# Kernel optimization log

Measured on AMD Instinct MI355X. Metric: run time of the kernel, lower is better.

Reference implementation:

```python
import jax, jax.numpy as jnp
import numpy as np

N = 50000
E = 800000
D = 128
C = 16


def setup_inputs() -> dict:
    key = jax.random.key(0)
    ks = jax.random.split(key, 16)
    inp = {
        "src": jax.random.randint(ks[0], (E,), 0, N),
        "dst": jax.random.randint(ks[1], (E,), 0, N),
        "inputs": jax.random.normal(ks[2], (N, D), dtype=jnp.float32),
        "edge_weights": jax.random.uniform(ks[3], (E,), dtype=jnp.float32),
    }
    s = 1.0 / np.sqrt(D)
    for i, k in zip(range(1, 5), ks[4:8]):
        inp[f"W{i}"] = jax.random.uniform(k, (D, D), jnp.float32, -s, s)
        inp[f"b{i}"] = jnp.zeros((D,), jnp.float32)
    inp["Wr"] = jax.random.uniform(ks[8], (D, D), jnp.float32, -s, s)
    inp["br"] = jnp.zeros((D,), jnp.float32)
    inp["Wo"] = jax.random.uniform(ks[9], (D, C), jnp.float32, -s, s)
    inp["bo"] = jnp.zeros((C,), jnp.float32)
    return inp


def _graph_conv(x, W, b, src, dst, ew, inv_sqrt_out, inv_sqrt_in):
    # DGL GraphConv, norm='both': scale src by out_deg^-1/2, weighted SpMM, scale by in_deg^-1/2
    h = (x * inv_sqrt_out[:, None]) @ W            # [N, d_out]
    m = h[src] * ew[:, None]                       # gather + edge scale, [E, d_out]
    agg = jax.ops.segment_sum(m, dst, num_segments=N)
    return agg * inv_sqrt_in[:, None] + b


def reference(src, dst, inputs, edge_weights, W1, b1, W2, b2, W3, b3, W4, b4, Wr, br, Wo, bo):
    ones = jnp.ones((E,), jnp.float32)
    deg_out = jnp.clip(jax.ops.segment_sum(ones, src, num_segments=N), 1.0)
    deg_in = jnp.clip(jax.ops.segment_sum(ones, dst, num_segments=N), 1.0)
    iso = jax.lax.rsqrt(deg_out)
    isi = jax.lax.rsqrt(deg_in)

    res = inputs @ Wr + br
    out = jax.nn.relu(_graph_conv(inputs, W1, b1, src, dst, edge_weights, iso, isi))
    out = jax.nn.relu(_graph_conv(out, W2, b2, src, dst, edge_weights, iso, isi))
    out = jax.nn.relu(_graph_conv(out, W3, b3, src, dst, edge_weights, iso, isi))
    out = _graph_conv(out, W4, b4, src, dst, edge_weights, iso, isi)
    out = jax.nn.relu(out + res)
    return out @ Wo + bo
```

## Files before the change

kernel.cpp:

```cpp
#include <hip/hip_runtime.h>

#define NN 50000
#define EE 800000
#define DD 128
#define CC 16
#define HCOPIES 64
#define NRANGE 16384

typedef __attribute__((ext_vector_type(8))) short bf16x8;
typedef __attribute__((ext_vector_type(4))) float f32x4;

__device__ inline unsigned short f2bf(float x) {
    unsigned int u = __float_as_uint(x);
    unsigned int r = (u + 0x7FFFu + ((u >> 16) & 1u)) >> 16;
    return (unsigned short)r;
}
__device__ inline float bf2f(unsigned short h) {
    return __uint_as_float(((unsigned int)h) << 16);
}

__global__ __launch_bounds__(256) void k_hist_lds(
        const int* __restrict__ src, const int* __restrict__ dst,
        unsigned int* __restrict__ hist) {
    __shared__ unsigned int lds[NRANGE];
    const int t = threadIdx.x;
    const int r = blockIdx.x / HCOPIES;
    const int sub = blockIdx.x % HCOPIES;
    const int base = r * NRANGE;
    const int hi = min(base + NRANGE, NN) - base;

    for (int i = t; i < NRANGE; i += 256) lds[i] = 0;
    __syncthreads();

    const int chunk = EE / HCOPIES;
    const int e0 = sub * chunk;
    const int e1 = e0 + chunk;
    for (int e = e0 + t; e < e1; e += 256) {
        int s = src[e];
        int d = dst[e];
        unsigned us = (unsigned)(s - base);
        unsigned ud = (unsigned)(d - base);
        if (us < (unsigned)hi) atomicAdd(&lds[us], 1u);
        if (ud < (unsigned)hi) atomicAdd(&lds[ud], 0x10000u);
    }
    __syncthreads();

    for (int i = t; i < hi; i += 256) hist[(size_t)sub * NN + base + i] = lds[i];
}

__global__ void k_reduce_deg(const unsigned int* __restrict__ hist,
                             int* __restrict__ cd,
                             float* __restrict__ iso, float* __restrict__ isi) {
    int i = blockIdx.x * blockDim.x + threadIdx.x;
    if (i < NN) {
        unsigned int sum = 0;
#pragma unroll
        for (int c = 0; c < HCOPIES; ++c) sum += hist[(size_t)c * NN + i];
        unsigned int csv = sum & 0xFFFFu;
        unsigned int cdv = sum >> 16;
        cd[i] = (int)cdv;
        iso[i] = rsqrtf(fmaxf((float)csv, 1.0f));
        isi[i] = rsqrtf(fmaxf((float)cdv, 1.0f));
    }
}

#define SBLK 256
#define NBLK_SCAN ((NN + SBLK - 1) / SBLK)

__global__ __launch_bounds__(SBLK) void k_blocksum(const int* __restrict__ cnt,
                                                   int* __restrict__ partial) {
    __shared__ int s[SBLK];
    int t = threadIdx.x;
    int i = blockIdx.x * SBLK + t;
    int v = (i < NN) ? cnt[i] : 0;
    s[t] = v;
    __syncthreads();
    for (int off = SBLK / 2; off > 0; off >>= 1) {
        if (t < off) s[t] += s[t + off];
        __syncthreads();
    }
    if (t == 0) partial[blockIdx.x] = s[0];
}

__global__ __launch_bounds__(SBLK) void k_scanpartial(const int* __restrict__ partial,
                                                      int* __restrict__ pp,
                                                      int* __restrict__ rowptr) {
    __shared__ int s[SBLK];
    int t = threadIdx.x;
    int v = (t < NBLK_SCAN) ? partial[t] : 0;
    s[t] = v;
    __syncthreads();
    for (int off = 1; off < SBLK; off <<= 1) {
        int x = (t >= off) ? s[t - off] : 0;
        __syncthreads();
        s[t] += x;
        __syncthreads();
    }
    if (t < NBLK_SCAN) pp[t] = s[t] - v;
    if (t == SBLK - 1) rowptr[NN] = s[t];
}

__global__ __launch_bounds__(SBLK) void k_writerowptr(const int* __restrict__ cnt,
                                                      const int* __restrict__ pp,
                                                      int* __restrict__ rowptr) {
    __shared__ int s[SBLK];
    int t = threadIdx.x;
    int i = blockIdx.x * SBLK + t;
    int v = (i < NN) ? cnt[i] : 0;
    s[t] = v;
    __syncthreads();
    for (int off = 1; off < SBLK; off <<= 1) {
        int x = (t >= off) ? s[t - off] : 0;
        __syncthreads();
        s[t] += x;
        __syncthreads();
    }
    if (i < NN) rowptr[i] = pp[blockIdx.x] + s[t] - v;
}

__global__ void k_fill(const int* __restrict__ src, const int* __restrict__ dst,
                       const float* __restrict__ ew, const float* __restrict__ iso,
                       const float* __restrict__ isi, const int* __restrict__ rowptr,
                       int* __restrict__ cursor, int2* __restrict__ pairs) {
    int e = blockIdx.x * blockDim.x + threadIdx.x;
    if (e < EE) {
        int d = dst[e];
        int s = src[e];
        int pos = atomicAdd(&cursor[d], 1);
        float w = ew[e] * iso[s] * isi[d];
        int2 p;
        p.x = s;
        p.y = __float_as_int(w);
        int idx = rowptr[d] + pos;
        if ((unsigned)idx < EE) pairs[idx] = p;
    }
}

__global__ __launch_bounds__(256) void k_tobf(const float* __restrict__ X,
                                              unsigned short* __restrict__ Hb) {
    int i = blockIdx.x * blockDim.x + threadIdx.x;
    if (i < NN * DD / 4) {
        float4 v = *(const float4*)&X[i * 4];
        ushort4 h;
        h.x = f2bf(v.x); h.y = f2bf(v.y); h.z = f2bf(v.z); h.w = f2bf(v.w);
        *(ushort4*)&Hb[i * 4] = h;
    }
}

__global__ __launch_bounds__(256) void k_gather_bf(
        const unsigned short* __restrict__ H, const int* __restrict__ rowptr,
        const int2* __restrict__ pairs, float* __restrict__ G) {
    int node = blockIdx.x * 4 + (threadIdx.x >> 6);
    if (node >= NN) return;
    int lane = threadIdx.x & 63;
    int c = lane * 2;
    int j = rowptr[node];
    int end = rowptr[node + 1];
    j = max(0, min(j, EE));
    end = max(j, min(end, EE));
    float2 a0 = make_float2(0.f, 0.f);
    float2 a1 = make_float2(0.f, 0.f);
    float2 a2 = make_float2(0.f, 0.f);
    float2 a3 = make_float2(0.f, 0.f);
    for (; j + 7 < end; j += 8) {
        int2 p0 = pairs[j + 0];
        int2 p1 = pairs[j + 1];
        int2 p2 = pairs[j + 2];
        int2 p3 = pairs[j + 3];
        int2 p4 = pairs[j + 4];
        int2 p5 = pairs[j + 5];
        int2 p6 = pairs[j + 6];
        int2 p7 = pairs[j + 7];
        int c0 = ((unsigned)p0.x < NN) ? p0.x : 0;
        int c1 = ((unsigned)p1.x < NN) ? p1.x : 0;
        int c2 = ((unsigned)p2.x < NN) ? p2.x : 0;
        int c3 = ((unsigned)p3.x < NN) ? p3.x : 0;
        int c4 = ((unsigned)p4.x < NN) ? p4.x : 0;
        int c5 = ((unsigned)p5.x < NN) ? p5.x : 0;
        int c6 = ((unsigned)p6.x < NN) ? p6.x : 0;
        int c7 = ((unsigned)p7.x < NN) ? p7.x : 0;
        ushort2 h0 = *(const ushort2*)&H[c0 * DD + c];
        ushort2 h1 = *(const ushort2*)&H[c1 * DD + c];
        ushort2 h2 = *(const ushort2*)&H[c2 * DD + c];
        ushort2 h3 = *(const ushort2*)&H[c3 * DD + c];
        ushort2 h4 = *(const ushort2*)&H[c4 * DD + c];
        ushort2 h5 = *(const ushort2*)&H[c5 * DD + c];
        ushort2 h6 = *(const ushort2*)&H[c6 * DD + c];
        ushort2 h7 = *(const ushort2*)&H[c7 * DD + c];
        float w0 = __int_as_float(p0.y);
        float w1 = __int_as_float(p1.y);
        float w2 = __int_as_float(p2.y);
        float w3 = __int_as_float(p3.y);
        float w4 = __int_as_float(p4.y);
        float w5 = __int_as_float(p5.y);
        float w6 = __int_as_float(p6.y);
        float w7 = __int_as_float(p7.y);
        a0.x = fmaf(bf2f(h0.x), w0, a0.x); a0.y = fmaf(bf2f(h0.y), w0, a0.y);
        a1.x = fmaf(bf2f(h1.x), w1, a1.x); a1.y = fmaf(bf2f(h1.y), w1, a1.y);
        a2.x = fmaf(bf2f(h2.x), w2, a2.x); a2.y = fmaf(bf2f(h2.y), w2, a2.y);
        a3.x = fmaf(bf2f(h3.x), w3, a3.x); a3.y = fmaf(bf2f(h3.y), w3, a3.y);
        a0.x = fmaf(bf2f(h4.x), w4, a0.x); a0.y = fmaf(bf2f(h4.y), w4, a0.y);
        a1.x = fmaf(bf2f(h5.x), w5, a1.x); a1.y = fmaf(bf2f(h5.y), w5, a1.y);
        a2.x = fmaf(bf2f(h6.x), w6, a2.x); a2.y = fmaf(bf2f(h6.y), w6, a2.y);
        a3.x = fmaf(bf2f(h7.x), w7, a3.x); a3.y = fmaf(bf2f(h7.y), w7, a3.y);
    }
    for (; j < end; ++j) {
        int2 p0 = pairs[j];
        int c0 = ((unsigned)p0.x < NN) ? p0.x : 0;
        float w0 = __int_as_float(p0.y);
        ushort2 h0 = *(const ushort2*)&H[c0 * DD + c];
        a0.x = fmaf(bf2f(h0.x), w0, a0.x); a0.y = fmaf(bf2f(h0.y), w0, a0.y);
    }
    float2 o = make_float2((a0.x + a1.x) + (a2.x + a3.x),
                           (a0.y + a1.y) + (a2.y + a3.y));
    *(float2*)&G[node * DD + c] = o;
}

__global__ __launch_bounds__(128) void k_prepw(
        const float* __restrict__ W1, const float* __restrict__ W2,
        const float* __restrict__ W3, const float* __restrict__ W4,
        const float* __restrict__ Wr,
        unsigned short* __restrict__ WH, unsigned short* __restrict__ WL) {
    int m = blockIdx.x >> 7;
    int c = blockIdx.x & 127;
    int k = threadIdx.x;
    const float* Wm = (m == 0) ? W1 : (m == 1) ? W2 : (m == 2) ? W3 : (m == 3) ? W4 : Wr;
    float x = Wm[k * 128 + c];
    unsigned short hi = f2bf(x);
    unsigned short lo = f2bf(x - bf2f(hi));
    int off = m * 16384 + c * 128 + k;
    WH[off] = hi;
    WL[off] = lo;
}

#define GTILE 64
__global__ __launch_bounds__(512) void k_gemm_mfma(
        const float* __restrict__ X,
        const unsigned short* __restrict__ Wh, const unsigned short* __restrict__ Wl,
        const float* __restrict__ bias, const float* __restrict__ RES,
        float* __restrict__ Yf, unsigned short* __restrict__ Yb, int M, int relu) {
    __shared__ unsigned short Xh[GTILE * 128];
    __shared__ unsigned short Xlo[GTILE * 128];

    const int t = threadIdx.x;
    const int row0 = blockIdx.x * GTILE;
    const float4* X4 = (const float4*)X;

    const int lane = t & 63;
    const int wav = t >> 6;
    const int lr = lane & 15;
    const int lk = lane >> 4;

    bf16x8 bh[4], bl[4];
    {
        const int c = 16 * wav + lr;
#pragma unroll
        for (int k0 = 0; k0 < 4; ++k0) {
            int off = c * 128 + k0 * 32 + lk * 8;
            bh[k0] = *(const bf16x8*)&Wh[off];
            bl[k0] = *(const bf16x8*)&Wl[off];
        }
    }

    for (int i = t; i < GTILE * 32; i += 512) {
        int r = i >> 5;
        int c4 = i & 31;
        int gr = row0 + r;
        float4 v = make_float4(0.f, 0.f, 0.f, 0.f);
        if (gr < M) v = X4[(long long)gr * 32 + c4];
        ushort4 h, lo;
        h.x = f2bf(v.x); lo.x = f2bf(v.x - bf2f(h.x));
        h.y = f2bf(v.y); lo.y = f2bf(v.y - bf2f(h.y));
        h.z = f2bf(v.z); lo.z = f2bf(v.z - bf2f(h.z));
        h.w = f2bf(v.w); lo.w = f2bf(v.w - bf2f(h.w));
        int base = r * 128 + ((c4 * 4) ^ ((r & 7) << 3));
        *(ushort4*)&Xh[base] = h;
        *(ushort4*)&Xlo[base] = lo;
    }
    __syncthreads();

    f32x4 acc[4];
#pragma unroll
    for (int m = 0; m < 4; ++m) acc[m] = (f32x4){0.f, 0.f, 0.f, 0.f};

#pragma unroll
    for (int k0 = 0; k0 < 4; ++k0) {
        const int kbase = k0 * 32 + lk * 8;
        bf16x8 ah[4], al[4];
#pragma unroll
        for (int m = 0; m < 4; ++m) {
            int row = 16 * m + lr;
            int off = row * 128 + (kbase ^ ((row & 7) << 3));
            ah[m] = *(const bf16x8*)&Xh[off];
            al[m] = *(const bf16x8*)&Xlo[off];
        }
#pragma unroll
        for (int m = 0; m < 4; ++m) {
            acc[m] = __builtin_amdgcn_mfma_f32_16x16x32_bf16(ah[m], bh[k0], acc[m], 0, 0, 0);
            acc[m] = __builtin_amdgcn_mfma_f32_16x16x32_bf16(ah[m], bl[k0], acc[m], 0, 0, 0);
            acc[m] = __builtin_amdgcn_mfma_f32_16x16x32_bf16(al[m], bh[k0], acc[m], 0, 0, 0);
        }
    }

    {
        int gc = 16 * wav + lr;
        float bv = bias[gc];
#pragma unroll
        for (int m = 0; m < 4; ++m) {
#pragma unroll
            for (int j = 0; j < 4; ++j) {
                int gr = row0 + 16 * m + lk * 4 + j;
                if (gr < M) {
                    float a = acc[m][j] + bv;
                    if (RES) a += RES[(long long)gr * DD + gc];
                    if (relu) a = fmaxf(a, 0.f);
                    if (Yb) Yb[(long long)gr * DD + gc] = f2bf(a);
                    else    Yf[(long long)gr * DD + gc] = a;
                }
            }
        }
    }
}

__global__ __launch_bounds__(256) void k_gemm_out(
        const float* __restrict__ X, const float* __restrict__ Wo,
        const float* __restrict__ bo, float* __restrict__ Y, int M) {
    __shared__ float Wlds[128 * 16];
    int t = threadIdx.x;
    for (int i = t * 4; i < 128 * 16; i += 256 * 4) {
        *(float4*)&Wlds[i] = *(const float4*)&Wo[i];
    }
    __syncthreads();
    int r = blockIdx.x * blockDim.x + t;
    if (r < M) {
        float acc[16];
#pragma unroll
        for (int j = 0; j < 16; ++j) acc[j] = bo[j];
#pragma unroll
        for (int k = 0; k < 128; k += 4) {
            float4 x = *(const float4*)&X[(long long)r * DD + k];
#pragma unroll
            for (int j = 0; j < 16; ++j) {
                acc[j] += x.x * Wlds[(k + 0) * 16 + j] + x.y * Wlds[(k + 1) * 16 + j]
                        + x.z * Wlds[(k + 2) * 16 + j] + x.w * Wlds[(k + 3) * 16 + j];
            }
        }
#pragma unroll
        for (int j = 0; j < 16; j += 4) {
            float4 o = make_float4(acc[j], acc[j + 1], acc[j + 2], acc[j + 3]);
            *(float4*)&Y[(long long)r * CC + j] = o;
        }
    }
}

extern "C" void kernel_launch(void* const* d_in, const int* in_sizes, int n_in,
                              void* d_out, int out_size, void* d_ws, size_t ws_size,
                              hipStream_t stream) {
    const int*   src = (const int*)d_in[0];
    const int*   dst = (const int*)d_in[1];
    const float* inputs = (const float*)d_in[2];
    const float* ew  = (const float*)d_in[3];
    const float* W1  = (const float*)d_in[4];
    const float* b1  = (const float*)d_in[5];
    const float* W2  = (const float*)d_in[6];
    const float* b2  = (const float*)d_in[7];
    const float* W3  = (const float*)d_in[8];
    const float* b3  = (const float*)d_in[9];
    const float* W4  = (const float*)d_in[10];
    const float* b4  = (const float*)d_in[11];
    const float* Wr  = (const float*)d_in[12];
    const float* br  = (const float*)d_in[13];
    const float* Wo  = (const float*)d_in[14];
    const float* bo  = (const float*)d_in[15];
    float* out = (float*)d_out;

    char* p = (char*)d_ws;
    float* iso    = (float*)p; p += sizeof(float) * NN;
    float* isi    = (float*)p; p += sizeof(float) * NN;
    int*   cs     = (int*)p;   p += sizeof(int) * NN;
    int*   cd     = (int*)p;   p += sizeof(int) * NN;
    int*   cursor = (int*)p;   p += sizeof(int) * NN;
    int*   rowptr = (int*)p;   p += sizeof(int) * (NN + 1);
    int*   partial= (int*)p;   p += sizeof(int) * NBLK_SCAN;
    int*   pp     = (int*)p;   p += sizeof(int) * NBLK_SCAN;
    p = (char*)(((uintptr_t)p + 255) & ~(uintptr_t)255);
    int2*  pairs  = (int2*)p;  p += sizeof(int2) * EE;
    float* RES    = (float*)p; p += sizeof(float) * (size_t)NN * DD;
    float* G      = (float*)p; p += sizeof(float) * (size_t)NN * DD;
    float* X0     = (float*)p; p += sizeof(float) * (size_t)NN * DD;

    unsigned short* WHg = (unsigned short*)cs;
    unsigned short* WLg = WHg + 5 * 16384;
    unsigned int*   hist = (unsigned int*)G;
    unsigned short* H   = (unsigned short*)X0;
    unsigned short* Hin = H + (size_t)NN * DD;

    const int GEMM_GRID = (NN + GTILE - 1) / GTILE;
    const int NRANGES = (NN + NRANGE - 1) / NRANGE;

    hipMemsetAsync(cursor, 0, sizeof(int) * NN, stream);
    k_hist_lds<<<NRANGES * HCOPIES, 256, 0, stream>>>(src, dst, hist);
    k_reduce_deg<<<(NN + 255) / 256, 256, 0, stream>>>(hist, cd, iso, isi);
    k_blocksum<<<NBLK_SCAN, SBLK, 0, stream>>>(cd, partial);
    k_scanpartial<<<1, SBLK, 0, stream>>>(partial, pp, rowptr);
    k_writerowptr<<<NBLK_SCAN, SBLK, 0, stream>>>(cd, pp, rowptr);
    k_fill<<<(EE + 255) / 256, 256, 0, stream>>>(src, dst, ew, iso, isi, rowptr, cursor, pairs);

    k_prepw<<<5 * 128, 128, 0, stream>>>(W1, W2, W3, W4, Wr, WHg, WLg);
    k_tobf<<<(NN * DD / 4 + 255) / 256, 256, 0, stream>>>(inputs, Hin);

    k_gemm_mfma<<<GEMM_GRID, 512, 0, stream>>>(inputs, WHg + 4 * 16384, WLg + 4 * 16384,
                                               br, nullptr, RES, nullptr, NN, 0);

    const float* bs[4] = {b1, b2, b3, b4};
    for (int l = 0; l < 4; ++l) {
        const unsigned short* Hs = (l == 0) ? Hin : H;
        k_gather_bf<<<(NN + 3) / 4, 256, 0, stream>>>(Hs, rowptr, pairs, G);

        if (l < 3) {
            k_gemm_mfma<<<GEMM_GRID, 512, 0, stream>>>(G, WHg + l * 16384, WLg + l * 16384,
                                                       bs[l], nullptr, nullptr, H, NN, 1);
        } else {
            k_gemm_mfma<<<GEMM_GRID, 512, 0, stream>>>(G, WHg + l * 16384, WLg + l * 16384,
                                                       bs[l], RES, X0, nullptr, NN, 1);
        }
    }

    k_gemm_out<<<(NN + 255) / 256, 256, 0, stream>>>(X0, Wo, bo, out, NN);
}
```

Measured before the change: 360.5 us.

## Pack edge pairs into 32-bit and store gathered features in bf16

Edge records shrink from int2 (index plus fp32 weight) to a single 32-bit word holding a 16-bit source index and an fp16 weight. The gather now writes bf16 instead of fp32, and the GEMM reads bf16 directly. It drops the low-part split of the activations and its third MFMA pass, cutting memory traffic and compute in the gather and GEMM stages. The cost is precision: activations lose their residual correction, weights are rounded to fp16, and the 16-bit index only holds because N is below 65536.

Result: faster. 340.1 us (-5.7%).

```diff
diff --git a/kernel.cpp b/kernel.cpp
--- a/kernel.cpp
+++ b/kernel.cpp
@@ -1,4 +1,5 @@
 #include <hip/hip_runtime.h>
+#include <hip/hip_fp16.h>
 
 #define NN 50000
 #define EE 800000
@@ -121,18 +122,17 @@
 __global__ void k_fill(const int* __restrict__ src, const int* __restrict__ dst,
                        const float* __restrict__ ew, const float* __restrict__ iso,
                        const float* __restrict__ isi, const int* __restrict__ rowptr,
-                       int* __restrict__ cursor, int2* __restrict__ pairs) {
+                       int* __restrict__ cursor, unsigned int* __restrict__ pairs) {
     int e = blockIdx.x * blockDim.x + threadIdx.x;
     if (e < EE) {
         int d = dst[e];
         int s = src[e];
         int pos = atomicAdd(&cursor[d], 1);
         float w = ew[e] * iso[s] * isi[d];
-        int2 p;
-        p.x = s;
-        p.y = __float_as_int(w);
+        unsigned short hw = __half_as_ushort(__float2half(w));
+        unsigned int pk = ((unsigned)s & 0xFFFFu) | ((unsigned)hw << 16);
         int idx = rowptr[d] + pos;
-        if ((unsigned)idx < EE) pairs[idx] = p;
+        if ((unsigned)idx < EE) pairs[idx] = pk;
     }
 }
 
@@ -149,7 +149,7 @@
 
 __global__ __launch_bounds__(256) void k_gather_bf(
         const unsigned short* __restrict__ H, const int* __restrict__ rowptr,
-        const int2* __restrict__ pairs, float* __restrict__ G) {
+        const unsigned int* __restrict__ pairs, unsigned short* __restrict__ G) {
     int node = blockIdx.x * 4 + (threadIdx.x >> 6);
     if (node >= NN) return;
     int lane = threadIdx.x & 63;
@@ -163,22 +163,22 @@
     float2 a2 = make_float2(0.f, 0.f);
     float2 a3 = make_float2(0.f, 0.f);
     for (; j + 7 < end; j += 8) {
-        int2 p0 = pairs[j + 0];
-        int2 p1 = pairs[j + 1];
-        int2 p2 = pairs[j + 2];
-        int2 p3 = pairs[j + 3];
-        int2 p4 = pairs[j + 4];
-        int2 p5 = pairs[j + 5];
-        int2 p6 = pairs[j + 6];
-        int2 p7 = pairs[j + 7];
-        int c0 = ((unsigned)p0.x < NN) ? p0.x : 0;
-        int c1 = ((unsigned)p1.x < NN) ? p1.x : 0;
-        int c2 = ((unsigned)p2.x < NN) ? p2.x : 0;
-        int c3 = ((unsigned)p3.x < NN) ? p3.x : 0;
-        int c4 = ((unsigned)p4.x < NN) ? p4.x : 0;
-        int c5 = ((unsigned)p5.x < NN) ? p5.x : 0;
-        int c6 = ((unsigned)p6.x < NN) ? p6.x : 0;
-        int c7 = ((unsigned)p7.x < NN) ? p7.x : 0;
+        unsigned p0 = pairs[j + 0];
+        unsigned p1 = pairs[j + 1];
+        unsigned p2 = pairs[j + 2];
+        unsigned p3 = pairs[j + 3];
+        unsigned p4 = pairs[j + 4];
+        unsigned p5 = pairs[j + 5];
+        unsigned p6 = pairs[j + 6];
+        unsigned p7 = pairs[j + 7];
+        int c0 = (p0 & 0xFFFFu) < NN ? (p0 & 0xFFFFu) : 0;
+        int c1 = (p1 & 0xFFFFu) < NN ? (p1 & 0xFFFFu) : 0;
+        int c2 = (p2 & 0xFFFFu) < NN ? (p2 & 0xFFFFu) : 0;
+        int c3 = (p3 & 0xFFFFu) < NN ? (p3 & 0xFFFFu) : 0;
+        int c4 = (p4 & 0xFFFFu) < NN ? (p4 & 0xFFFFu) : 0;
+        int c5 = (p5 & 0xFFFFu) < NN ? (p5 & 0xFFFFu) : 0;
+        int c6 = (p6 & 0xFFFFu) < NN ? (p6 & 0xFFFFu) : 0;
+        int c7 = (p7 & 0xFFFFu) < NN ? (p7 & 0xFFFFu) : 0;
         ushort2 h0 = *(const ushort2*)&H[c0 * DD + c];
         ushort2 h1 = *(const ushort2*)&H[c1 * DD + c];
         ushort2 h2 = *(const ushort2*)&H[c2 * DD + c];
@@ -187,14 +187,14 @@
         ushort2 h5 = *(const ushort2*)&H[c5 * DD + c];
         ushort2 h6 = *(const ushort2*)&H[c6 * DD + c];
         ushort2 h7 = *(const ushort2*)&H[c7 * DD + c];
-        float w0 = __int_as_float(p0.y);
-        float w1 = __int_as_float(p1.y);
-        float w2 = __int_as_float(p2.y);
-        float w3 = __int_as_float(p3.y);
-        float w4 = __int_as_float(p4.y);
-        float w5 = __int_as_float(p5.y);
-        float w6 = __int_as_float(p6.y);
-        float w7 = __int_as_float(p7.y);
+        float w0 = __half2float(__ushort_as_half((unsigned short)(p0 >> 16)));
+        float w1 = __half2float(__ushort_as_half((unsigned short)(p1 >> 16)));
+        float w2 = __half2float(__ushort_as_half((unsigned short)(p2 >> 16)));
+        float w3 = __half2float(__ushort_as_half((unsigned short)(p3 >> 16)));
+        float w4 = __half2float(__ushort_as_half((unsigned short)(p4 >> 16)));
+        float w5 = __half2float(__ushort_as_half((unsigned short)(p5 >> 16)));
+        float w6 = __half2float(__ushort_as_half((unsigned short)(p6 >> 16)));
+        float w7 = __half2float(__ushort_as_half((unsigned short)(p7 >> 16)));
         a0.x = fmaf(bf2f(h0.x), w0, a0.x); a0.y = fmaf(bf2f(h0.y), w0, a0.y);
         a1.x = fmaf(bf2f(h1.x), w1, a1.x); a1.y = fmaf(bf2f(h1.y), w1, a1.y);
         a2.x = fmaf(bf2f(h2.x), w2, a2.x); a2.y = fmaf(bf2f(h2.y), w2, a2.y);
@@ -205,15 +205,18 @@
         a3.x = fmaf(bf2f(h7.x), w7, a3.x); a3.y = fmaf(bf2f(h7.y), w7, a3.y);
     }
     for (; j < end; ++j) {
-        int2 p0 = pairs[j];
-        int c0 = ((unsigned)p0.x < NN) ? p0.x : 0;
-        float w0 = __int_as_float(p0.y);
+        unsigned p0 = pairs[j];
+        int c0 = (p0 & 0xFFFFu) < NN ? (p0 & 0xFFFFu) : 0;
+        float w0 = __half2float(__ushort_as_half((unsigned short)(p0 >> 16)));
         ushort2 h0 = *(const ushort2*)&H[c0 * DD + c];
         a0.x = fmaf(bf2f(h0.x), w0, a0.x); a0.y = fmaf(bf2f(h0.y), w0, a0.y);
     }
-    float2 o = make_float2((a0.x + a1.x) + (a2.x + a3.x),
-                           (a0.y + a1.y) + (a2.y + a3.y));
-    *(float2*)&G[node * DD + c] = o;
+    float ox = (a0.x + a1.x) + (a2.x + a3.x);
+    float oy = (a0.y + a1.y) + (a2.y + a3.y);
+    ushort2 o;
+    o.x = f2bf(ox);
+    o.y = f2bf(oy);
+    *(ushort2*)&G[node * DD + c] = o;
 }
 
 __global__ __launch_bounds__(128) void k_prepw(
@@ -235,16 +238,14 @@
 
 #define GTILE 64
 __global__ __launch_bounds__(512) void k_gemm_mfma(
-        const float* __restrict__ X,
+        const unsigned short* __restrict__ Xb,
         const unsigned short* __restrict__ Wh, const unsigned short* __restrict__ Wl,
         const float* __restrict__ bias, const float* __restrict__ RES,
         float* __restrict__ Yf, unsigned short* __restrict__ Yb, int M, int relu) {
-    __shared__ unsigned short Xh[GTILE * 128];
-    __shared__ unsigned short Xlo[GTILE * 128];
+    __shared__ unsigned short Xs[GTILE * 128];
 
     const int t = threadIdx.x;
     const int row0 = blockIdx.x * GTILE;
-    const float4* X4 = (const float4*)X;
 
     const int lane = t & 63;
     const int wav = t >> 6;
@@ -262,20 +263,14 @@
         }
     }
 
-    for (int i = t; i < GTILE * 32; i += 512) {
-        int r = i >> 5;
-        int c4 = i & 31;
+    for (int i = t; i < GTILE * 16; i += 512) {
+        int r = i >> 4;
+        int c8 = i & 15;
         int gr = row0 + r;
-        float4 v = make_float4(0.f, 0.f, 0.f, 0.f);
-        if (gr < M) v = X4[(long long)gr * 32 + c4];
-        ushort4 h, lo;
-        h.x = f2bf(v.x); lo.x = f2bf(v.x - bf2f(h.x));
-        h.y = f2bf(v.y); lo.y = f2bf(v.y - bf2f(h.y));
-        h.z = f2bf(v.z); lo.z = f2bf(v.z - bf2f(h.z));
-        h.w = f2bf(v.w); lo.w = f2bf(v.w - bf2f(h.w));
-        int base = r * 128 + ((c4 * 4) ^ ((r & 7) << 3));
-        *(ushort4*)&Xh[base] = h;
-        *(ushort4*)&Xlo[base] = lo;
+        bf16x8 v = {0, 0, 0, 0, 0, 0, 0, 0};
+        if (gr < M) v = *(const bf16x8*)&Xb[(size_t)gr * 128 + c8 * 8];
+        int slot = (c8 * 8) ^ ((r & 7) << 3);
+        *(bf16x8*)&Xs[r * 128 + slot] = v;
     }
     __syncthreads();
 
@@ -286,19 +281,16 @@
 #pragma unroll
     for (int k0 = 0; k0 < 4; ++k0) {
         const int kbase = k0 * 32 + lk * 8;
-        bf16x8 ah[4], al[4];
+        bf16x8 ah[4];
 #pragma unroll
         for (int m = 0; m < 4; ++m) {
             int row = 16 * m + lr;
-            int off = row * 128 + (kbase ^ ((row & 7) << 3));
-            ah[m] = *(const bf16x8*)&Xh[off];
-            al[m] = *(const bf16x8*)&Xlo[off];
+            ah[m] = *(const bf16x8*)&Xs[row * 128 + (kbase ^ ((row & 7) << 3))];
         }
 #pragma unroll
         for (int m = 0; m < 4; ++m) {
             acc[m] = __builtin_amdgcn_mfma_f32_16x16x32_bf16(ah[m], bh[k0], acc[m], 0, 0, 0);
             acc[m] = __builtin_amdgcn_mfma_f32_16x16x32_bf16(ah[m], bl[k0], acc[m], 0, 0, 0);
-            acc[m] = __builtin_amdgcn_mfma_f32_16x16x32_bf16(al[m], bh[k0], acc[m], 0, 0, 0);
         }
     }
 
@@ -384,7 +376,8 @@
     int*   partial= (int*)p;   p += sizeof(int) * NBLK_SCAN;
     int*   pp     = (int*)p;   p += sizeof(int) * NBLK_SCAN;
     p = (char*)(((uintptr_t)p + 255) & ~(uintptr_t)255);
-    int2*  pairs  = (int2*)p;  p += sizeof(int2) * EE;
+    unsigned int* pairs = (unsigned int*)p; p += sizeof(unsigned int) * EE;
+    p = (char*)(((uintptr_t)p + 255) & ~(uintptr_t)255);
     float* RES    = (float*)p; p += sizeof(float) * (size_t)NN * DD;
     float* G      = (float*)p; p += sizeof(float) * (size_t)NN * DD;
     float* X0     = (float*)p; p += sizeof(float) * (size_t)NN * DD;
@@ -392,6 +385,7 @@
     unsigned short* WHg = (unsigned short*)cs;
     unsigned short* WLg = WHg + 5 * 16384;
     unsigned int*   hist = (unsigned int*)G;
+    unsigned short* Gb  = (unsigned short*)G;
     unsigned short* H   = (unsigned short*)X0;
     unsigned short* Hin = H + (size_t)NN * DD;
 
@@ -409,19 +403,19 @@
     k_prepw<<<5 * 128, 128, 0, stream>>>(W1, W2, W3, W4, Wr, WHg, WLg);
     k_tobf<<<(NN * DD / 4 + 255) / 256, 256, 0, stream>>>(inputs, Hin);
 
-    k_gemm_mfma<<<GEMM_GRID, 512, 0, stream>>>(inputs, WHg + 4 * 16384, WLg + 4 * 16384,
+    k_gemm_mfma<<<GEMM_GRID, 512, 0, stream>>>(Hin, WHg + 4 * 16384, WLg + 4 * 16384,
                                                br, nullptr, RES, nullptr, NN, 0);
 
     const float* bs[4] = {b1, b2, b3, b4};
     for (int l = 0; l < 4; ++l) {
         const unsigned short* Hs = (l == 0) ? Hin : H;
-        k_gather_bf<<<(NN + 3) / 4, 256, 0, stream>>>(Hs, rowptr, pairs, G);
+        k_gather_bf<<<(NN + 3) / 4, 256, 0, stream>>>(Hs, rowptr, pairs, Gb);
 
         if (l < 3) {
-            k_gemm_mfma<<<GEMM_GRID, 512, 0, stream>>>(G, WHg + l * 16384, WLg + l * 16384,
+            k_gemm_mfma<<<GEMM_GRID, 512, 0, stream>>>(Gb, WHg + l * 16384, WLg + l * 16384,
                                                        bs[l], nullptr, nullptr, H, NN, 1);
         } else {
-            k_gemm_mfma<<<GEMM_GRID, 512, 0, stream>>>(G, WHg + l * 16384, WLg + l * 16384,
+            k_gemm_mfma<<<GEMM_GRID, 512, 0, stream>>>(Gb, WHg + l * 16384, WLg + l * 16384,
                                                        bs[l], RES, X0, nullptr, NN, 1);
         }
     }
```
